# Kernel optimization log

Measured on AMD Instinct MI355X. Metric: run time of the kernel, lower is better.

The kernel has to match this reference:

```python
import jax, jax.numpy as jnp
import numpy as np

N_NODES = 100000
N_EDGES = 3200000
N_FEAT = 512
N_CLASS = 10
HIDDEN = 16
EPS = 1e-12  # matches torch F.normalize clamp


def setup_inputs() -> dict:
    key = jax.random.key(0)
    ks = jax.random.split(key, 6)
    x = jax.random.normal(ks[0], (N_NODES, N_FEAT), dtype=jnp.float32)
    edge_index = jax.random.randint(ks[1], (2, N_EDGES), 0, N_NODES, dtype=jnp.int64)
    W1 = jax.random.normal(ks[2], (N_FEAT, HIDDEN), dtype=jnp.float32) / np.sqrt(N_FEAT)
    b1 = jnp.zeros((HIDDEN,), dtype=jnp.float32)
    beta = jnp.ones((1,), dtype=jnp.float32)  # learnable scalar of prop2
    W2 = jax.random.normal(ks[3], (HIDDEN, N_CLASS), dtype=jnp.float32) / np.sqrt(HIDDEN)
    b2 = jnp.zeros((N_CLASS,), dtype=jnp.float32)
    return {"x": x, "edge_index": edge_index, "W1": W1, "b1": b1,
            "beta": beta, "W2": W2, "b2": b2}


def _agnn_conv(h, src, dst, beta_val, n_nodes):
    # L2-normalize node features (cosine attention)
    norm = jnp.maximum(jnp.linalg.norm(h, axis=-1, keepdims=True), EPS)
    hn = h / norm
    # per-edge attention logit: beta * cos(h_i, h_j)
    alpha = beta_val * jnp.sum(hn[src] * hn[dst], axis=-1)  # [E]
    # scatter-softmax over edges sharing the same destination node
    amax = jax.ops.segment_max(alpha, dst, num_segments=n_nodes)
    ea = jnp.exp(alpha - amax[dst])
    denom = jax.ops.segment_sum(ea, dst, num_segments=n_nodes)
    w = ea / denom[dst]  # self-loops guarantee denom > 0
    # weighted aggregation of source features into destination nodes
    return jax.ops.segment_sum(w[:, None] * h[src], dst, num_segments=n_nodes)


def reference(x, edge_index, W1, b1, beta, W2, b2):
    n = x.shape[0]
    # dropout is identity in eval mode
    h = jax.nn.relu(x @ W1 + b1)  # [N, 16]
    # AGNNConv adds self-loops before propagation
    loops = jnp.arange(n, dtype=edge_index.dtype)
    src = jnp.concatenate([edge_index[0], loops])
    dst = jnp.concatenate([edge_index[1], loops])
    h = _agnn_conv(h, src, dst, jnp.float32(1.0), n)   # prop1: beta fixed to 1
    h = _agnn_conv(h, src, dst, beta[0], n)            # prop2: learnable beta
    logits = h @ W2 + b2
    return jax.nn.log_softmax(logits, axis=-1)
```

## Files before the change

kernel.cpp:

```cpp
#include <hip/hip_runtime.h>
#include <hip/hip_fp16.h>
#include <math.h>

#define N_NODES 100000
#define N_EDGES 3200000
#define EPRIME  (N_EDGES + N_NODES)
#define NFEAT   512
#define HID     16
#define NCLS    10

#define NPB     256
#define NB      ((N_NODES + NPB - 1) / NPB)
#define CHUNK   4096
#define NCHUNKS ((EPRIME + CHUNK - 1) / CHUNK)
#define CAPB    10240
#define CAP     12288

union U2 { unsigned int u; __half2 h; };
__device__ __forceinline__ float2 u2f(unsigned int v) {
  U2 t; t.u = v; return __half22float2(t.h);
}

__global__ __launch_bounds__(256) void k_gemm_norm(const float* __restrict__ x,
                                                   const float* __restrict__ W1,
                                                   const float* __restrict__ b1,
                                                   __half* __restrict__ hn1,
                                                   float* __restrict__ norms1,
                                                   int* __restrict__ gcur) {
  if (blockIdx.x == 0)
    for (int i = threadIdx.x; i < NB; i += 256) gcur[i] = 0;

  const int lane = threadIdx.x & 63;
  const int wid  = blockIdx.x * 4 + (threadIdx.x >> 6);
  const int nw   = gridDim.x * 4;

  float4 w[8][4];
#pragma unroll
  for (int kk = 0; kk < 8; ++kk)
#pragma unroll
    for (int j = 0; j < 4; ++j)
      w[kk][j] = *reinterpret_cast<const float4*>(W1 + (lane * 8 + kk) * 16 + j * 4);

  const int outCol = (lane >> 2) & 15;
  const float bias = b1[outCol];

  const float4 z4 = make_float4(0.f, 0.f, 0.f, 0.f);
  float4 c0 = z4, c1 = z4, p0 = z4, p1 = z4, t0 = z4, t1 = z4;

  if (wid < N_NODES) {
    c0 = *reinterpret_cast<const float4*>(x + (size_t)wid * NFEAT + lane * 8);
    c1 = *reinterpret_cast<const float4*>(x + (size_t)wid * NFEAT + lane * 8 + 4);
  }
  if (wid + nw < N_NODES) {
    p0 = *reinterpret_cast<const float4*>(x + (size_t)(wid + nw) * NFEAT + lane * 8);
    p1 = *reinterpret_cast<const float4*>(x + (size_t)(wid + nw) * NFEAT + lane * 8 + 4);
  }

  for (int row = wid; row < N_NODES; row += nw) {
    const int r2 = row + 2 * nw;
    if (r2 < N_NODES) {
      t0 = *reinterpret_cast<const float4*>(x + (size_t)r2 * NFEAT + lane * 8);
      t1 = *reinterpret_cast<const float4*>(x + (size_t)r2 * NFEAT + lane * 8 + 4);
    }

    float xs[8] = {c0.x, c0.y, c0.z, c0.w, c1.x, c1.y, c1.z, c1.w};

    float acc[16];
#pragma unroll
    for (int j = 0; j < 16; ++j) acc[j] = 0.f;

#pragma unroll
    for (int kk = 0; kk < 8; ++kk) {
      const float xv = xs[kk];
#pragma unroll
      for (int j4 = 0; j4 < 4; ++j4) {
        acc[j4 * 4 + 0] = fmaf(xv, w[kk][j4].x, acc[j4 * 4 + 0]);
        acc[j4 * 4 + 1] = fmaf(xv, w[kk][j4].y, acc[j4 * 4 + 1]);
        acc[j4 * 4 + 2] = fmaf(xv, w[kk][j4].z, acc[j4 * 4 + 2]);
        acc[j4 * 4 + 3] = fmaf(xv, w[kk][j4].w, acc[j4 * 4 + 3]);
      }
    }

#pragma unroll
    for (int i = 0; i < 8; ++i) {
      float send = (lane & 32) ? acc[i] : acc[i + 8];
      float r = __shfl_xor(send, 32);
      acc[i] = ((lane & 32) ? acc[i + 8] : acc[i]) + r;
    }
#pragma unroll
    for (int i = 0; i < 4; ++i) {
      float send = (lane & 16) ? acc[i] : acc[i + 4];
      float r = __shfl_xor(send, 16);
      acc[i] = ((lane & 16) ? acc[i + 4] : acc[i]) + r;
    }
#pragma unroll
    for (int i = 0; i < 2; ++i) {
      float send = (lane & 8) ? acc[i] : acc[i + 2];
      float r = __shfl_xor(send, 8);
      acc[i] = ((lane & 8) ? acc[i + 2] : acc[i]) + r;
    }
    {
      float send = (lane & 4) ? acc[0] : acc[1];
      float r = __shfl_xor(send, 4);
      acc[0] = ((lane & 4) ? acc[1] : acc[0]) + r;
    }
    acc[0] += __shfl_xor(acc[0], 2);
    acc[0] += __shfl_xor(acc[0], 1);

    const float v = fmaxf(acc[0] + bias, 0.f);
    float ss = v * v;
    ss += __shfl_xor(ss, 4);
    ss += __shfl_xor(ss, 8);
    ss += __shfl_xor(ss, 16);
    ss += __shfl_xor(ss, 32);
    const float nrm = sqrtf(ss);
    const float vs = v / fmaxf(nrm, 1e-12f);

    const float wv = __shfl(vs, (lane & 15) * 4);
    if (lane < 16) hn1[(size_t)row * HID + lane] = __float2half_rn(wv);
    if (lane == 0) norms1[row] = nrm;

    c0 = p0; c1 = p1; p0 = t0; p1 = t1;
  }
}

__global__ __launch_bounds__(256) void k_part(const int* __restrict__ ei,
                                              int* __restrict__ gcur,
                                              unsigned int* __restrict__ slots) {
  __shared__ int hist[NB];
  __shared__ int gbase[NB];
  for (int i = threadIdx.x; i < NB; i += 256) hist[i] = 0;
  __syncthreads();

  const int base = blockIdx.x * CHUNK;
  unsigned int pk[CHUNK / 256];
  int bk[CHUNK / 256];
  int rk[CHUNK / 256];
#pragma unroll
  for (int j = 0; j < CHUNK / 256; ++j) {
    int e = base + j * 256 + threadIdx.x;
    bool valid = (e < EPRIME);
    int srcv = 0, d = 0;
    if (valid) {
      if (e < N_EDGES) { srcv = ei[e]; d = ei[N_EDGES + e]; }
      else             { srcv = d = e - N_EDGES; }
    }
    bk[j] = valid ? (d >> 8) : -1;
    pk[j] = (unsigned)srcv | ((unsigned)(d & 255) << 20);
    rk[j] = valid ? atomicAdd(&hist[d >> 8], 1) : 0;
  }
  __syncthreads();

  for (int i = threadIdx.x; i < NB; i += 256) {
    int hc = hist[i];
    gbase[i] = hc ? atomicAdd(&gcur[i], hc) : 0;
  }
  __syncthreads();

#pragma unroll
  for (int j = 0; j < CHUNK / 256; ++j)
    if (bk[j] >= 0) slots[(size_t)bk[j] * CAPB + gbase[bk[j]] + rk[j]] = pk[j];
}

__global__ void k_bscan(const int* __restrict__ gcur, int* __restrict__ boffs,
                        int* __restrict__ offs, int* __restrict__ csr) {
  __shared__ int s[512];
  const int t = threadIdx.x;
  int v = (t < NB) ? gcur[t] : 0;
  s[t] = v;
  __syncthreads();
  for (int d = 1; d < 512; d <<= 1) {
    int u = (t >= d) ? s[t - d] : 0;
    __syncthreads();
    s[t] += u;
    __syncthreads();
  }
  if (t < NB) boffs[t] = s[t] - v;
  if (t == 0) offs[N_NODES] = EPRIME;
  if (t >= 480 && t < 496) csr[EPRIME + (t - 480)] = 0;
}

__global__ __launch_bounds__(256) void k_csr(const unsigned int* __restrict__ slots,
                                             const int* __restrict__ boffs,
                                             const int* __restrict__ gcur,
                                             int* __restrict__ offs,
                                             int* __restrict__ csr) {
  __shared__ int cnt[NPB];
  __shared__ int cnt2[NPB];
  __shared__ int sc[NPB];
  __shared__ int loffs[NPB];
  __shared__ int srcb[CAP];

  const int b = blockIdx.x;
  const int base = boffs[b];
  const int ne = gcur[b];
  const int t = threadIdx.x;
  const unsigned int* my = slots + (size_t)b * CAPB;

  cnt[t] = 0;
  cnt2[t] = 0;
  __syncthreads();

  for (int i = t; i < ne; i += 256) atomicAdd(&cnt[my[i] >> 20], 1);
  __syncthreads();

  int v = cnt[t];
  sc[t] = v;
  __syncthreads();
  for (int d = 1; d < NPB; d <<= 1) {
    int u = (t >= d) ? sc[t - d] : 0;
    __syncthreads();
    sc[t] += u;
    __syncthreads();
  }
  int excl = sc[t] - v;
  loffs[t] = excl;

  const int node = b * NPB + t;
  if (node < N_NODES) offs[node] = base + excl;
  __syncthreads();

  if (ne <= CAP) {
    for (int i = t; i < ne; i += 256) {
      unsigned p = my[i];
      int local = p >> 20;
      int r = atomicAdd(&cnt2[local], 1);
      srcb[loffs[local] + r] = (int)(p & 0xFFFFF);
    }
    __syncthreads();
    for (int i = t; i < ne; i += 256) csr[base + i] = srcb[i];
  } else {
    for (int i = t; i < ne; i += 256) {
      unsigned p = my[i];
      int local = p >> 20;
      int r = atomicAdd(&cnt2[local], 1);
      csr[base + loffs[local] + r] = (int)(p & 0xFFFFF);
    }
  }
}

template <bool FINAL>
__global__ __launch_bounds__(256) void k_pull(const __half* __restrict__ hn,
                                              const float* __restrict__ norms,
                                              const int* __restrict__ offs,
                                              const int* __restrict__ csr,
                                              const float* __restrict__ beta_ptr,
                                              __half* __restrict__ out_hn,
                                              float* __restrict__ out_norms,
                                              float* __restrict__ h3) {
  const int node = blockIdx.x * 4 + (threadIdx.x >> 6);
  if (node >= N_NODES) return;
  const int lane = threadIdx.x & 63;
  const int q    = lane & 3;
  const int slot = lane >> 2;
  const float beta = FINAL ? beta_ptr[0] : 1.0f;

  const uint2 qraw = *reinterpret_cast<const uint2*>(hn + (size_t)node * HID + q * 4);
  const float2 qa = u2f(qraw.x), qb = u2f(qraw.y);
  const int s = offs[node], e = offs[node + 1];

  float den = 0.f;
  float ax = 0.f, ay = 0.f, az = 0.f, aw = 0.f;

  for (int b2 = s; b2 < e; b2 += 16) {
    const int i = b2 + slot;
    const int src = csr[i];
    const uint2 r = *reinterpret_cast<const uint2*>(hn + (size_t)src * HID + q * 4);
    const float2 f0 = u2f(r.x), f1 = u2f(r.y);
    float pd = qa.x * f0.x + qa.y * f0.y + qb.x * f1.x + qb.y * f1.y;
    pd += __shfl_xor(pd, 1);
    pd += __shfl_xor(pd, 2);
    const float t = (i < e) ? __expf(beta * pd) : 0.f;
    den += t;
    const float wgt = t * norms[src];
    ax += wgt * f0.x; ay += wgt * f0.y; az += wgt * f1.x; aw += wgt * f1.y;
  }

#pragma unroll
  for (int m = 4; m <= 32; m <<= 1) {
    den += __shfl_xor(den, m);
    ax  += __shfl_xor(ax, m);
    ay  += __shfl_xor(ay, m);
    az  += __shfl_xor(az, m);
    aw  += __shfl_xor(aw, m);
  }
  const float inv = 1.0f / den;
  ax *= inv; ay *= inv; az *= inv; aw *= inv;

  if (!FINAL) {
    float ssn = ax * ax + ay * ay + az * az + aw * aw;
    ssn += __shfl_xor(ssn, 1);
    ssn += __shfl_xor(ssn, 2);
    const float nrm = sqrtf(ssn);
    const float ninv = 1.0f / fmaxf(nrm, 1e-12f);
    if (lane < 4) {
      U2 lo, hi;
      lo.h = __floats2half2_rn(ax * ninv, ay * ninv);
      hi.h = __floats2half2_rn(az * ninv, aw * ninv);
      *reinterpret_cast<uint2*>(out_hn + (size_t)node * HID + q * 4) =
          make_uint2(lo.u, hi.u);
      if (lane == 0) out_norms[node] = nrm;
    }
  } else {
    if (lane < 4)
      *reinterpret_cast<float4*>(h3 + (size_t)node * HID + q * 4) =
          make_float4(ax, ay, az, aw);
  }
}

__global__ void k_out(const float* __restrict__ h, const float* __restrict__ W2,
                      const float* __restrict__ b2, float* __restrict__ out) {
  int n = blockIdx.x * blockDim.x + threadIdx.x;
  if (n >= N_NODES) return;
  const float4* hp = reinterpret_cast<const float4*>(h + (size_t)n * HID);
  const float4 h0 = hp[0], h1 = hp[1], h2 = hp[2], h3 = hp[3];
  const float hv[16] = {h0.x, h0.y, h0.z, h0.w, h1.x, h1.y, h1.z, h1.w,
                        h2.x, h2.y, h2.z, h2.w, h3.x, h3.y, h3.z, h3.w};
  float lg[10];
#pragma unroll
  for (int c = 0; c < NCLS; ++c) {
    float s = b2[c];
#pragma unroll
    for (int j = 0; j < HID; ++j) s = fmaf(hv[j], W2[j * NCLS + c], s);
    lg[c] = s;
  }
  float m = lg[0];
#pragma unroll
  for (int c = 1; c < NCLS; ++c) m = fmaxf(m, lg[c]);
  float se = 0.f;
#pragma unroll
  for (int c = 0; c < NCLS; ++c) se += __expf(lg[c] - m);
  const float ls = m + logf(se);
#pragma unroll
  for (int c = 0; c < NCLS; ++c) out[(size_t)n * NCLS + c] = lg[c] - ls;
}

extern "C" void kernel_launch(void* const* d_in, const int* in_sizes, int n_in,
                              void* d_out, int out_size, void* d_ws, size_t ws_size,
                              hipStream_t stream) {
  const float* x    = (const float*)d_in[0];
  const int*   ei   = (const int*)d_in[1];
  const float* W1   = (const float*)d_in[2];
  const float* b1   = (const float*)d_in[3];
  const float* beta = (const float*)d_in[4];
  const float* W2   = (const float*)d_in[5];
  const float* b2   = (const float*)d_in[6];
  float* out = (float*)d_out;

  float*  base   = (float*)d_ws;
  __half* hn1    = (__half*)base;
  float*  norms1 = base + (size_t)N_NODES * 8;
  __half* hn2    = (__half*)(norms1 + N_NODES);
  float*  norms2 = (float*)(hn2 + (size_t)N_NODES * HID);
  float*  h3     = norms2 + N_NODES;
  int*    offs   = (int*)(h3 + (size_t)N_NODES * HID);
  int*    gcur   = offs + N_NODES + 8;
  int*    boffs  = gcur + NB;
  int*    csr    = boffs + NB;
  unsigned int* slots = (unsigned int*)(csr + EPRIME + 16);

  k_gemm_norm<<<1024, 256, 0, stream>>>(x, W1, b1, hn1, norms1, gcur);

  k_part<<<NCHUNKS, 256, 0, stream>>>(ei, gcur, slots);
  k_bscan<<<1, 512, 0, stream>>>(gcur, boffs, offs, csr);
  k_csr<<<NB, 256, 0, stream>>>(slots, boffs, gcur, offs, csr);

  const int nblW = (N_NODES + 3) / 4;

  k_pull<false><<<nblW, 256, 0, stream>>>(hn1, norms1, offs, csr, nullptr,
                                          hn2, norms2, nullptr);
  k_pull<true><<<nblW, 256, 0, stream>>>(hn2, norms2, offs, csr, beta,
                                         nullptr, nullptr, h3);

  k_out<<<(N_NODES + 255) / 256, 256, 0, stream>>>(h3, W2, b2, out);
}
```

Measured before the change: 258.0 us.

## Merge CSR build and both propagations into one cooperative persistent kernel

Replaces the partition, scan, CSR build, two pull passes and output kernel with a single cooperative kernel that uses grid.sync between phases, falling back to separate launches if cooperative launch is unavailable. The block-offset scan is folded into each CSR block as a partial sum over gcur, and the final linear layer plus log-softmax is fused into the second pull pass, dropping the h3 buffer. The CSR build no longer stages through a shared-memory buffer and scatters straight to global memory. The aim is to remove launch gaps and intermediate traffic, at the cost of a fixed 768-block persistent grid that may limit occupancy and parallelism in the pull phases.

Measured after the change: 656.6 us. 2.54x slower.

```diff
diff --git a/kernel.cpp b/kernel.cpp
--- a/kernel.cpp
+++ b/kernel.cpp
@@ -1,6 +1,9 @@
 #include <hip/hip_runtime.h>
 #include <hip/hip_fp16.h>
+#include <hip/hip_cooperative_groups.h>
 #include <math.h>
+
+namespace cg = cooperative_groups;
 
 #define N_NODES 100000
 #define N_EDGES 3200000
@@ -14,7 +17,7 @@
 #define CHUNK   4096
 #define NCHUNKS ((EPRIME + CHUNK - 1) / CHUNK)
 #define CAPB    10240
-#define CAP     12288
+#define GRID2   768
 
 union U2 { unsigned int u; __half2 h; };
 __device__ __forceinline__ float2 u2f(unsigned int v) {
@@ -124,21 +127,23 @@
   }
 }
 
-__global__ __launch_bounds__(256) void k_part(const int* __restrict__ ei,
-                                              int* __restrict__ gcur,
-                                              unsigned int* __restrict__ slots) {
-  __shared__ int hist[NB];
-  __shared__ int gbase[NB];
-  for (int i = threadIdx.x; i < NB; i += 256) hist[i] = 0;
-  __syncthreads();
-
-  const int base = blockIdx.x * CHUNK;
+__device__ void part_chunk(int c, const int* __restrict__ ei,
+                           int* __restrict__ gcur,
+                           unsigned int* __restrict__ slots) {
+  __shared__ int sh_hist[NB];
+  __shared__ int sh_gbase[NB];
+  const int tid = threadIdx.x;
+
+  for (int i = tid; i < NB; i += 256) sh_hist[i] = 0;
+  __syncthreads();
+
+  const int base = c * CHUNK;
   unsigned int pk[CHUNK / 256];
   int bk[CHUNK / 256];
   int rk[CHUNK / 256];
 #pragma unroll
   for (int j = 0; j < CHUNK / 256; ++j) {
-    int e = base + j * 256 + threadIdx.x;
+    int e = base + j * 256 + tid;
     bool valid = (e < EPRIME);
     int srcv = 0, d = 0;
     if (valid) {
@@ -147,192 +152,241 @@
     }
     bk[j] = valid ? (d >> 8) : -1;
     pk[j] = (unsigned)srcv | ((unsigned)(d & 255) << 20);
-    rk[j] = valid ? atomicAdd(&hist[d >> 8], 1) : 0;
-  }
-  __syncthreads();
-
-  for (int i = threadIdx.x; i < NB; i += 256) {
-    int hc = hist[i];
-    gbase[i] = hc ? atomicAdd(&gcur[i], hc) : 0;
+    rk[j] = valid ? atomicAdd(&sh_hist[d >> 8], 1) : 0;
+  }
+  __syncthreads();
+
+  for (int i = tid; i < NB; i += 256) {
+    int hc = sh_hist[i];
+    sh_gbase[i] = hc ? atomicAdd(&gcur[i], hc) : 0;
   }
   __syncthreads();
 
 #pragma unroll
   for (int j = 0; j < CHUNK / 256; ++j)
-    if (bk[j] >= 0) slots[(size_t)bk[j] * CAPB + gbase[bk[j]] + rk[j]] = pk[j];
-}
-
-__global__ void k_bscan(const int* __restrict__ gcur, int* __restrict__ boffs,
-                        int* __restrict__ offs, int* __restrict__ csr) {
-  __shared__ int s[512];
-  const int t = threadIdx.x;
-  int v = (t < NB) ? gcur[t] : 0;
-  s[t] = v;
-  __syncthreads();
-  for (int d = 1; d < 512; d <<= 1) {
-    int u = (t >= d) ? s[t - d] : 0;
+    if (bk[j] >= 0)
+      slots[(size_t)bk[j] * CAPB + sh_gbase[bk[j]] + rk[j]] = pk[j];
+}
+
+__device__ void csr_finalize(int bid, const unsigned int* __restrict__ slots,
+                             const int* __restrict__ gcur,
+                             int* __restrict__ offs, int* __restrict__ csr) {
+  const int tid = threadIdx.x;
+  if (bid == NB) {
+    if (tid == 0) offs[N_NODES] = EPRIME;
+    if (tid < 16) csr[EPRIME + tid] = 0;
+    return;
+  }
+
+  __shared__ int sh_cnt[NPB];
+  __shared__ int sh_cnt2[NPB];
+  __shared__ int sh_sc[NPB];
+  __shared__ int sh_loffs[NPB];
+  __shared__ int sh_w[4];
+
+  int partial = 0;
+  for (int i = tid; i < bid; i += 256) partial += gcur[i];
+#pragma unroll
+  for (int m = 1; m < 64; m <<= 1) partial += __shfl_xor(partial, m);
+  if ((tid & 63) == 0) sh_w[tid >> 6] = partial;
+  sh_cnt[tid] = 0;
+  sh_cnt2[tid] = 0;
+  __syncthreads();
+
+  const int base = sh_w[0] + sh_w[1] + sh_w[2] + sh_w[3];
+  const int ne = gcur[bid];
+  const unsigned int* my = slots + (size_t)bid * CAPB;
+
+  for (int i = tid; i < ne; i += 256) atomicAdd(&sh_cnt[my[i] >> 20], 1);
+  __syncthreads();
+
+  int v = sh_cnt[tid];
+  sh_sc[tid] = v;
+  __syncthreads();
+  for (int d = 1; d < NPB; d <<= 1) {
+    int u = (tid >= d) ? sh_sc[tid - d] : 0;
     __syncthreads();
-    s[t] += u;
+    sh_sc[tid] += u;
     __syncthreads();
   }
-  if (t < NB) boffs[t] = s[t] - v;
-  if (t == 0) offs[N_NODES] = EPRIME;
-  if (t >= 480 && t < 496) csr[EPRIME + (t - 480)] = 0;
-}
-
-__global__ __launch_bounds__(256) void k_csr(const unsigned int* __restrict__ slots,
-                                             const int* __restrict__ boffs,
-                                             const int* __restrict__ gcur,
-                                             int* __restrict__ offs,
-                                             int* __restrict__ csr) {
-  __shared__ int cnt[NPB];
-  __shared__ int cnt2[NPB];
-  __shared__ int sc[NPB];
-  __shared__ int loffs[NPB];
-  __shared__ int srcb[CAP];
-
-  const int b = blockIdx.x;
-  const int base = boffs[b];
-  const int ne = gcur[b];
-  const int t = threadIdx.x;
-  const unsigned int* my = slots + (size_t)b * CAPB;
-
-  cnt[t] = 0;
-  cnt2[t] = 0;
-  __syncthreads();
-
-  for (int i = t; i < ne; i += 256) atomicAdd(&cnt[my[i] >> 20], 1);
-  __syncthreads();
-
-  int v = cnt[t];
-  sc[t] = v;
-  __syncthreads();
-  for (int d = 1; d < NPB; d <<= 1) {
-    int u = (t >= d) ? sc[t - d] : 0;
-    __syncthreads();
-    sc[t] += u;
-    __syncthreads();
-  }
-  int excl = sc[t] - v;
-  loffs[t] = excl;
-
-  const int node = b * NPB + t;
+  const int excl = sh_sc[tid] - v;
+  sh_loffs[tid] = excl;
+
+  const int node = bid * NPB + tid;
   if (node < N_NODES) offs[node] = base + excl;
   __syncthreads();
 
-  if (ne <= CAP) {
-    for (int i = t; i < ne; i += 256) {
-      unsigned p = my[i];
-      int local = p >> 20;
-      int r = atomicAdd(&cnt2[local], 1);
-      srcb[loffs[local] + r] = (int)(p & 0xFFFFF);
-    }
-    __syncthreads();
-    for (int i = t; i < ne; i += 256) csr[base + i] = srcb[i];
-  } else {
-    for (int i = t; i < ne; i += 256) {
-      unsigned p = my[i];
-      int local = p >> 20;
-      int r = atomicAdd(&cnt2[local], 1);
-      csr[base + loffs[local] + r] = (int)(p & 0xFFFFF);
-    }
+  for (int i = tid; i < ne; i += 256) {
+    unsigned p = my[i];
+    int local = p >> 20;
+    int r = atomicAdd(&sh_cnt2[local], 1);
+    csr[base + sh_loffs[local] + r] = (int)(p & 0xFFFFF);
   }
 }
 
 template <bool FINAL>
-__global__ __launch_bounds__(256) void k_pull(const __half* __restrict__ hn,
-                                              const float* __restrict__ norms,
-                                              const int* __restrict__ offs,
-                                              const int* __restrict__ csr,
-                                              const float* __restrict__ beta_ptr,
-                                              __half* __restrict__ out_hn,
-                                              float* __restrict__ out_norms,
-                                              float* __restrict__ h3) {
-  const int node = blockIdx.x * 4 + (threadIdx.x >> 6);
-  if (node >= N_NODES) return;
+__device__ __forceinline__ void pull_body(const __half* __restrict__ hn,
+                                          const float* __restrict__ norms,
+                                          const int* __restrict__ offs,
+                                          const int* __restrict__ csr,
+                                          float beta,
+                                          __half* __restrict__ out_hn,
+                                          float* __restrict__ out_norms,
+                                          const float* __restrict__ W2,
+                                          const float* __restrict__ b2,
+                                          float* __restrict__ out,
+                                          int wid0, int stride) {
   const int lane = threadIdx.x & 63;
   const int q    = lane & 3;
   const int slot = lane >> 2;
-  const float beta = FINAL ? beta_ptr[0] : 1.0f;
-
-  const uint2 qraw = *reinterpret_cast<const uint2*>(hn + (size_t)node * HID + q * 4);
-  const float2 qa = u2f(qraw.x), qb = u2f(qraw.y);
-  const int s = offs[node], e = offs[node + 1];
-
-  float den = 0.f;
-  float ax = 0.f, ay = 0.f, az = 0.f, aw = 0.f;
-
-  for (int b2 = s; b2 < e; b2 += 16) {
-    const int i = b2 + slot;
-    const int src = csr[i];
-    const uint2 r = *reinterpret_cast<const uint2*>(hn + (size_t)src * HID + q * 4);
-    const float2 f0 = u2f(r.x), f1 = u2f(r.y);
-    float pd = qa.x * f0.x + qa.y * f0.y + qb.x * f1.x + qb.y * f1.y;
-    pd += __shfl_xor(pd, 1);
-    pd += __shfl_xor(pd, 2);
-    const float t = (i < e) ? __expf(beta * pd) : 0.f;
-    den += t;
-    const float wgt = t * norms[src];
-    ax += wgt * f0.x; ay += wgt * f0.y; az += wgt * f1.x; aw += wgt * f1.y;
-  }
-
-#pragma unroll
-  for (int m = 4; m <= 32; m <<= 1) {
-    den += __shfl_xor(den, m);
-    ax  += __shfl_xor(ax, m);
-    ay  += __shfl_xor(ay, m);
-    az  += __shfl_xor(az, m);
-    aw  += __shfl_xor(aw, m);
-  }
-  const float inv = 1.0f / den;
-  ax *= inv; ay *= inv; az *= inv; aw *= inv;
-
-  if (!FINAL) {
-    float ssn = ax * ax + ay * ay + az * az + aw * aw;
-    ssn += __shfl_xor(ssn, 1);
-    ssn += __shfl_xor(ssn, 2);
-    const float nrm = sqrtf(ssn);
-    const float ninv = 1.0f / fmaxf(nrm, 1e-12f);
-    if (lane < 4) {
-      U2 lo, hi;
-      lo.h = __floats2half2_rn(ax * ninv, ay * ninv);
-      hi.h = __floats2half2_rn(az * ninv, aw * ninv);
-      *reinterpret_cast<uint2*>(out_hn + (size_t)node * HID + q * 4) =
-          make_uint2(lo.u, hi.u);
-      if (lane == 0) out_norms[node] = nrm;
-    }
-  } else {
-    if (lane < 4)
-      *reinterpret_cast<float4*>(h3 + (size_t)node * HID + q * 4) =
-          make_float4(ax, ay, az, aw);
-  }
-}
-
-__global__ void k_out(const float* __restrict__ h, const float* __restrict__ W2,
-                      const float* __restrict__ b2, float* __restrict__ out) {
-  int n = blockIdx.x * blockDim.x + threadIdx.x;
-  if (n >= N_NODES) return;
-  const float4* hp = reinterpret_cast<const float4*>(h + (size_t)n * HID);
-  const float4 h0 = hp[0], h1 = hp[1], h2 = hp[2], h3 = hp[3];
-  const float hv[16] = {h0.x, h0.y, h0.z, h0.w, h1.x, h1.y, h1.z, h1.w,
-                        h2.x, h2.y, h2.z, h2.w, h3.x, h3.y, h3.z, h3.w};
-  float lg[10];
-#pragma unroll
-  for (int c = 0; c < NCLS; ++c) {
-    float s = b2[c];
-#pragma unroll
-    for (int j = 0; j < HID; ++j) s = fmaf(hv[j], W2[j * NCLS + c], s);
-    lg[c] = s;
-  }
-  float m = lg[0];
-#pragma unroll
-  for (int c = 1; c < NCLS; ++c) m = fmaxf(m, lg[c]);
-  float se = 0.f;
-#pragma unroll
-  for (int c = 0; c < NCLS; ++c) se += __expf(lg[c] - m);
-  const float ls = m + logf(se);
-#pragma unroll
-  for (int c = 0; c < NCLS; ++c) out[(size_t)n * NCLS + c] = lg[c] - ls;
+
+  float w4x = 0.f, w4y = 0.f, w4z = 0.f, w4w = 0.f, b2v = 0.f;
+  if (FINAL) {
+    const int sc = (slot < NCLS) ? slot : 0;
+    w4x = W2[(q * 4 + 0) * NCLS + sc];
+    w4y = W2[(q * 4 + 1) * NCLS + sc];
+    w4z = W2[(q * 4 + 2) * NCLS + sc];
+    w4w = W2[(q * 4 + 3) * NCLS + sc];
+    b2v = b2[sc];
+  }
+
+  for (int node = wid0; node < N_NODES; node += stride) {
+    const uint2 qraw = *reinterpret_cast<const uint2*>(hn + (size_t)node * HID + q * 4);
+    const float2 qa = u2f(qraw.x), qb = u2f(qraw.y);
+    const int s = offs[node], e = offs[node + 1];
+
+    float den = 0.f;
+    float ax = 0.f, ay = 0.f, az = 0.f, aw = 0.f;
+
+    for (int bi = s; bi < e; bi += 16) {
+      const int i = bi + slot;
+      const int src = csr[i];
+      const uint2 r = *reinterpret_cast<const uint2*>(hn + (size_t)src * HID + q * 4);
+      const float2 f0 = u2f(r.x), f1 = u2f(r.y);
+      float pd = qa.x * f0.x + qa.y * f0.y + qb.x * f1.x + qb.y * f1.y;
+      pd += __shfl_xor(pd, 1);
+      pd += __shfl_xor(pd, 2);
+      const float t = (i < e) ? __expf(beta * pd) : 0.f;
+      den += t;
+      const float wgt = t * norms[src];
+      ax += wgt * f0.x; ay += wgt * f0.y; az += wgt * f1.x; aw += wgt * f1.y;
+    }
+
+#pragma unroll
+    for (int m = 4; m <= 32; m <<= 1) {
+      den += __shfl_xor(den, m);
+      ax  += __shfl_xor(ax, m);
+      ay  += __shfl_xor(ay, m);
+      az  += __shfl_xor(az, m);
+      aw  += __shfl_xor(aw, m);
+    }
+    const float inv = 1.0f / den;
+    ax *= inv; ay *= inv; az *= inv; aw *= inv;
+
+    if (!FINAL) {
+      float ssn = ax * ax + ay * ay + az * az + aw * aw;
+      ssn += __shfl_xor(ssn, 1);
+      ssn += __shfl_xor(ssn, 2);
+      const float nrm = sqrtf(ssn);
+      const float ninv = 1.0f / fmaxf(nrm, 1e-12f);
+      if (lane < 4) {
+        U2 lo, hi;
+        lo.h = __floats2half2_rn(ax * ninv, ay * ninv);
+        hi.h = __floats2half2_rn(az * ninv, aw * ninv);
+        *reinterpret_cast<uint2*>(out_hn + (size_t)node * HID + q * 4) =
+            make_uint2(lo.u, hi.u);
+        if (lane == 0) out_norms[node] = nrm;
+      }
+    } else {
+      float part = ax * w4x + ay * w4y + az * w4z + aw * w4w;
+      part += __shfl_xor(part, 1);
+      part += __shfl_xor(part, 2);
+      const float logit = part + b2v;
+
+      float lg[NCLS];
+#pragma unroll
+      for (int c = 0; c < NCLS; ++c) lg[c] = __shfl(logit, c * 4);
+      float m = lg[0];
+#pragma unroll
+      for (int c = 1; c < NCLS; ++c) m = fmaxf(m, lg[c]);
+      float se = 0.f;
+#pragma unroll
+      for (int c = 0; c < NCLS; ++c) se += __expf(lg[c] - m);
+      const float ls = m + logf(se);
+
+      const float myv = __shfl(logit, lane * 4);
+      if (lane < NCLS) out[(size_t)node * NCLS + lane] = myv - ls;
+    }
+  }
+}
+
+__global__ __launch_bounds__(256, 4) void k_mega(const int* __restrict__ ei,
+                                                 const float* __restrict__ beta_ptr,
+                                                 const __half* __restrict__ hn1,
+                                                 const float* __restrict__ norms1,
+                                                 __half* __restrict__ hn2,
+                                                 float* __restrict__ norms2,
+                                                 int* __restrict__ gcur,
+                                                 int* __restrict__ offs,
+                                                 int* __restrict__ csr,
+                                                 unsigned int* __restrict__ slots,
+                                                 const float* __restrict__ W2,
+                                                 const float* __restrict__ b2,
+                                                 float* __restrict__ out) {
+  cg::grid_group grid = cg::this_grid();
+  const int bid  = blockIdx.x;
+  const int wid0 = bid * 4 + (threadIdx.x >> 6);
+
+  for (int c = bid; c < NCHUNKS; c += GRID2)
+    part_chunk(c, ei, gcur, slots);
+  grid.sync();
+
+  if (bid <= NB)
+    csr_finalize(bid, slots, gcur, offs, csr);
+  grid.sync();
+
+  pull_body<false>(hn1, norms1, offs, csr, 1.0f, hn2, norms2,
+                   nullptr, nullptr, nullptr, wid0, GRID2 * 4);
+  grid.sync();
+
+  pull_body<true>(hn2, norms2, offs, csr, beta_ptr[0], nullptr, nullptr,
+                  W2, b2, out, wid0, GRID2 * 4);
+}
+
+__global__ __launch_bounds__(256) void k_part(const int* __restrict__ ei,
+                                              int* __restrict__ gcur,
+                                              unsigned int* __restrict__ slots) {
+  part_chunk(blockIdx.x, ei, gcur, slots);
+}
+
+__global__ __launch_bounds__(256) void k_csrfin(const unsigned int* __restrict__ slots,
+                                                const int* __restrict__ gcur,
+                                                int* __restrict__ offs,
+                                                int* __restrict__ csr) {
+  csr_finalize(blockIdx.x, slots, gcur, offs, csr);
+}
+
+__global__ __launch_bounds__(256) void k_pull1(const __half* __restrict__ hn1,
+                                               const float* __restrict__ norms1,
+                                               const int* __restrict__ offs,
+                                               const int* __restrict__ csr,
+                                               __half* __restrict__ hn2,
+                                               float* __restrict__ norms2) {
+  pull_body<false>(hn1, norms1, offs, csr, 1.0f, hn2, norms2,
+                   nullptr, nullptr, nullptr,
+                   blockIdx.x * 4 + (threadIdx.x >> 6), gridDim.x * 4);
+}
+
+__global__ __launch_bounds__(256) void k_pull2(const __half* __restrict__ hn2,
+                                               const float* __restrict__ norms2,
+                                               const int* __restrict__ offs,
+                                               const int* __restrict__ csr,
+                                               const float* __restrict__ beta_ptr,
+                                               const float* __restrict__ W2,
+                                               const float* __restrict__ b2,
+                                               float* __restrict__ out) {
+  pull_body<true>(hn2, norms2, offs, csr, beta_ptr[0], nullptr, nullptr,
+                  W2, b2, out, blockIdx.x * 4 + (threadIdx.x >> 6), gridDim.x * 4);
 }
 
 extern "C" void kernel_launch(void* const* d_in, const int* in_sizes, int n_in,
@@ -352,25 +406,31 @@
   float*  norms1 = base + (size_t)N_NODES * 8;
   __half* hn2    = (__half*)(norms1 + N_NODES);
   float*  norms2 = (float*)(hn2 + (size_t)N_NODES * HID);
-  float*  h3     = norms2 + N_NODES;
-  int*    offs   = (int*)(h3 + (size_t)N_NODES * HID);
+  int*    offs   = (int*)(norms2 + N_NODES);
   int*    gcur   = offs + N_NODES + 8;
-  int*    boffs  = gcur + NB;
-  int*    csr    = boffs + NB;
+  int*    csr    = gcur + NB + 1;
   unsigned int* slots = (unsigned int*)(csr + EPRIME + 16);
 
   k_gemm_norm<<<1024, 256, 0, stream>>>(x, W1, b1, hn1, norms1, gcur);
 
-  k_part<<<NCHUNKS, 256, 0, stream>>>(ei, gcur, slots);
-  k_bscan<<<1, 512, 0, stream>>>(gcur, boffs, offs, csr);
-  k_csr<<<NB, 256, 0, stream>>>(slots, boffs, gcur, offs, csr);
-
-  const int nblW = (N_NODES + 3) / 4;
-
-  k_pull<false><<<nblW, 256, 0, stream>>>(hn1, norms1, offs, csr, nullptr,
-                                          hn2, norms2, nullptr);
-  k_pull<true><<<nblW, 256, 0, stream>>>(hn2, norms2, offs, csr, beta,
-                                         nullptr, nullptr, h3);
-
-  k_out<<<(N_NODES + 255) / 256, 256, 0, stream>>>(h3, W2, b2, out);
-}
+  int maxB = 0;
+  hipError_t oe = hipOccupancyMaxActiveBlocksPerMultiprocessor(&maxB, k_mega, 256, 0);
+  bool coop = (oe == hipSuccess) && (maxB * 256 >= GRID2);
+
+  if (coop) {
+    void* args[] = {(void*)&ei, (void*)&beta, (void*)&hn1, (void*)&norms1,
+                    (void*)&hn2, (void*)&norms2, (void*)&gcur, (void*)&offs,
+                    (void*)&csr, (void*)&slots, (void*)&W2, (void*)&b2,
+                    (void*)&out};
+    hipError_t le = hipLaunchCooperativeKernel((void*)k_mega, dim3(GRID2),
+                                               dim3(256), args, 0, stream);
+    if (le != hipSuccess) { (void)hipGetLastError(); coop = false; }
+  }
+
+  if (!coop) {
+    k_part<<<NCHUNKS, 256, 0, stream>>>(ei, gcur, slots);
+    k_csrfin<<<NB + 1, 256, 0, stream>>>(slots, gcur, offs, csr);
+    k_pull1<<<6250, 256, 0, stream>>>(hn1, norms1, offs, csr, hn2, norms2);
+    k_pull2<<<6250, 256, 0, stream>>>(hn2, norms2, offs, csr, beta, W2, b2, out);
+  }
+}
```
